# Performance work log

Hardware: AMD Instinct MI355X
Metric: run time of the kernel (lower is better)

The kernel has to match this reference:

```python
import jax, jax.numpy as jnp
import numpy as np

EPS = 1e-5

def setup_inputs() -> dict:
    key = jax.random.key(0)
    ks = jax.random.split(key, 5)
    B, C_clip, Hc, Wc = 8, 768, 24, 24
    C_rs, Hr, Wr = 256, 64, 64
    clip_feat = jax.random.normal(ks[0], (B, C_clip, Hc, Wc), dtype=jnp.float32)
    rs_feat = jax.random.normal(ks[1], (B, C_rs, Hr, Wr), dtype=jnp.float32)
    ln_gamma = jnp.ones((C_clip,), dtype=jnp.float32)
    ln_beta = jnp.zeros((C_clip,), dtype=jnp.float32)
    W = jax.random.normal(ks[2], (C_rs, C_clip), dtype=jnp.float32) * (1.0 / np.sqrt(C_clip))
    b = jax.random.normal(ks[3], (C_rs,), dtype=jnp.float32) * 0.01
    alpha = jnp.array([0.5], dtype=jnp.float32)
    return {"clip_feat": clip_feat, "rs_feat": rs_feat, "ln_gamma": ln_gamma,
            "ln_beta": ln_beta, "W": W, "b": b, "alpha": alpha}

def reference(clip_feat, rs_feat, ln_gamma, ln_beta, W, b, alpha):
    B, C_clip, Hc, Wc = clip_feat.shape
    _, C_rs, Hr, Wr = rs_feat.shape
    # tokens: [B, N_clip, C_clip]
    clip_flat = clip_feat.reshape(B, C_clip, Hc * Wc).transpose(0, 2, 1)
    mu = jnp.mean(clip_flat, axis=-1, keepdims=True)
    var = jnp.var(clip_flat, axis=-1, keepdims=True)
    clip_norm = (clip_flat - mu) * jax.lax.rsqrt(var + EPS) * ln_gamma + ln_beta
    # projection to rs_dim: [B, N_clip, C_rs]
    clip_proj = jnp.einsum('bnc,dc->bnd', clip_norm, W) + b
    # rs tokens: [B, N_rs, C_rs]
    rs_flat = rs_feat.reshape(B, C_rs, Hr * Wr).transpose(0, 2, 1)
    # attn_map: [B, N_clip, N_rs], softmax over N_clip (axis=1)
    attn = jnp.einsum('bnd,bmd->bnm', clip_proj, rs_flat)
    attn = jax.nn.softmax(attn, axis=1)
    # attended: [B, N_rs, C_rs]
    attended = jnp.einsum('bnm,bnd->bmd', attn, clip_proj)
    attended = attended.transpose(0, 2, 1).reshape(B, C_rs, Hr, Wr)
    return rs_feat + alpha * attended
```

## Files before the change

### kernel.cpp

```cpp
#include <hip/hip_runtime.h>
#include <hip/hip_bf16.h>

#define EPSF 1e-5f
#define SM_OFF 60.0f

typedef short short8 __attribute__((ext_vector_type(8)));
typedef float f32x4 __attribute__((ext_vector_type(4)));

__device__ __forceinline__ short f2bf(float x) {
    __hip_bfloat16 h = __float2bfloat16(x);
    return reinterpret_cast<short&>(h);
}
__device__ __forceinline__ float bf2f(short s) {
    __hip_bfloat16 h = reinterpret_cast<__hip_bfloat16&>(s);
    return __bfloat162float(h);
}
__device__ __forceinline__ unsigned int pk2(float lo, float hi) {
    return (unsigned int)(unsigned short)f2bf(lo)
         | ((unsigned int)(unsigned short)f2bf(hi) << 16);
}
__device__ __forceinline__ void gload_lds16(const short* g, short* lds) {
    __builtin_amdgcn_global_load_lds(
        (const __attribute__((address_space(1))) unsigned int*)g,
        (__attribute__((address_space(3))) unsigned int*)lds,
        16, 0, 0);
}

__global__ __launch_bounds__(256) void w_pack_kernel(
    const float* __restrict__ W,
    short* __restrict__ Wp_hi,
    short* __restrict__ Wp_lo)
{
    int t = blockIdx.x * 256 + threadIdx.x;
    int l15 = t & 15;
    int g   = (t >> 4) & 3;
    int kt  = (t >> 6) % 24;
    int nt  = t / 1536;
    const float* src = W + (size_t)(16 * nt + l15) * 768 + 32 * kt + 8 * g;
    short8 h8, l8;
    #pragma unroll
    for (int j = 0; j < 8; ++j) {
        float w = src[j];
        short h = f2bf(w);
        h8[j] = h;
        l8[j] = f2bf(w - bf2f(h));
    }
    *reinterpret_cast<short8*>(Wp_hi + (size_t)t * 8) = h8;
    *reinterpret_cast<short8*>(Wp_lo + (size_t)t * 8) = l8;
}

__global__ __launch_bounds__(512) void ln_proj_kernel(
    const float* __restrict__ clip,
    const float* __restrict__ gamma,
    const float* __restrict__ beta,
    const short* __restrict__ Wp_hi,
    const short* __restrict__ Wp_lo,
    const float* __restrict__ bias,
    short* __restrict__ proj,
    short* __restrict__ projT)
{
    __shared__ short xh[16][776];
    __shared__ short xl[16][776];
    __shared__ float redA[8][16];
    __shared__ float redB[8][16];
    __shared__ float muS[16], rsS[16];

    const int tid = threadIdx.x;
    const int bb = blockIdx.x >> 1;
    const int dh = blockIdx.x & 1;
    const int b  = bb / 36;
    const int n0 = (bb % 36) * 16;
    const int nl = tid & 15;
    const int cg = tid >> 4;
    const int w  = tid >> 6;
    const int l  = tid & 63;
    const int l15 = l & 15;
    const int g  = l >> 4;

    const float* base = clip + (size_t)b * 768 * 576 + n0 + nl;

    float x[24];
    float s1 = 0.f, s2 = 0.f;
    #pragma unroll
    for (int i = 0; i < 24; ++i) {
        x[i] = base[(size_t)(cg + 32 * i) * 576];
        s1 += x[i]; s2 += x[i] * x[i];
    }
    s1 += __shfl_xor(s1, 16); s2 += __shfl_xor(s2, 16);
    s1 += __shfl_xor(s1, 32); s2 += __shfl_xor(s2, 32);
    if (g == 0) { redA[w][l15] = s1; redB[w][l15] = s2; }
    __syncthreads();
    if (tid < 16) {
        float a = 0.f, q = 0.f;
        #pragma unroll
        for (int k = 0; k < 8; ++k) { a += redA[k][tid]; q += redB[k][tid]; }
        float mu = a * (1.f / 768.f);
        float var = q * (1.f / 768.f) - mu * mu;
        muS[tid] = mu; rsS[tid] = rsqrtf(var + EPSF);
    }
    __syncthreads();
    {
        float mu = muS[nl], rsg = rsS[nl];
        #pragma unroll
        for (int i = 0; i < 24; ++i) {
            int c = cg + 32 * i;
            float y = (x[i] - mu) * rsg * gamma[c] + beta[c];
            short hh = f2bf(y);
            xh[nl][c] = hh;
            xl[nl][c] = f2bf(y - bf2f(hh));
        }
    }
    __syncthreads();

    const int nt = 8 * dh + w;
    f32x4 acc = f32x4{0.f, 0.f, 0.f, 0.f};
    for (int kt = 0; kt < 24; ++kt) {
        short8 ah = *reinterpret_cast<const short8*>(&xh[l15][32 * kt + 8 * g]);
        short8 al = *reinterpret_cast<const short8*>(&xl[l15][32 * kt + 8 * g]);
        size_t off = ((size_t)((nt * 24 + kt) * 64 + l)) * 8;
        short8 bh = *reinterpret_cast<const short8*>(Wp_hi + off);
        short8 bl = *reinterpret_cast<const short8*>(Wp_lo + off);
        acc = __builtin_amdgcn_mfma_f32_16x16x32_bf16(ah, bh, acc, 0, 0, 0);
        acc = __builtin_amdgcn_mfma_f32_16x16x32_bf16(al, bh, acc, 0, 0, 0);
        acc = __builtin_amdgcn_mfma_f32_16x16x32_bf16(ah, bl, acc, 0, 0, 0);
    }

    {
        int d = 16 * nt + l15;
        float bb2 = bias[d];
        #pragma unroll
        for (int r = 0; r < 4; ++r) {
            int tok = n0 + 4 * g + r;
            short v = f2bf(acc[r] + bb2);
            proj[((size_t)b * 576 + tok) * 256 + d] = v;
            projT[((size_t)b * 256 + d) * 576 + tok] = v;
        }
    }
}

__global__ __launch_bounds__(256, 2) void attn_kernel(
    const short* __restrict__ proj,
    const short* __restrict__ projT,
    const float* __restrict__ rs,
    const float* __restrict__ alpha_p,
    float* __restrict__ out)
{
    __shared__ short Ks[64][256];
    __shared__ short VT[256][64];
    __shared__ unsigned int Ps[4][16][36];

    const int tid = threadIdx.x;
    const int b  = blockIdx.x & 7;
    const int q0 = (blockIdx.x >> 3) << 6;
    const int w   = tid >> 6;
    const int l   = tid & 63;
    const int l15 = l & 15;
    const int g   = l >> 4;
    const int qg  = q0 + 16 * w + l15;

    const short* kbase  = proj  + (size_t)b * 576 * 256;
    const short* ktbase = projT + (size_t)b * 256 * 576;
    const float* rbase  = rs + (size_t)b * 256 * 4096;
    float* obase = out + (size_t)b * 256 * 4096;

    short8 qf[8];
    #pragma unroll
    for (int dc = 0; dc < 8; ++dc) {
        short8 v;
        #pragma unroll
        for (int j = 0; j < 8; ++j)
            v[j] = f2bf(rbase[(size_t)(32 * dc + 8 * g + j) * 4096 + qg]);
        qf[dc] = v;
    }

    f32x4 acc[16];
    #pragma unroll
    for (int dt = 0; dt < 16; ++dt) acc[dt] = f32x4{0.f, 0.f, 0.f, 0.f};
    float rsum = 0.f;

    auto STAGE = [&](int c) {
        #pragma unroll
        for (int i = 0; i < 8; ++i) {
            int row0 = 16 * w + 2 * i;
            int rr = row0 + (l >> 5);
            const short* src = kbase + ((size_t)(64 * c + rr) << 8)
                             + ((((l & 31) ^ (rr & 7))) << 3);
            gload_lds16(src, &Ks[row0][0]);
        }
        #pragma unroll
        for (int i = 0; i < 8; ++i) {
            int d0 = 64 * w + 8 * i;
            int d = d0 + (l >> 3);
            const short* src = ktbase + (size_t)d * 576 + 64 * c
                             + (((l & 7) ^ (d & 7)) << 3);
            gload_lds16(src, &VT[d0][0]);
        }
    };

    STAGE(0);
    __syncthreads();

    for (int c = 0; c < 9; ++c) {
        f32x4 s[4];
        #pragma unroll
        for (int kt = 0; kt < 4; ++kt) s[kt] = f32x4{0.f, 0.f, 0.f, 0.f};
        __builtin_amdgcn_s_setprio(1);
        #pragma unroll
        for (int dc = 0; dc < 8; ++dc) {
            int sw = (((4 * dc + g) ^ (l15 & 7))) * 8;
            #pragma unroll
            for (int kt = 0; kt < 4; ++kt) {
                short8 kf = *reinterpret_cast<const short8*>(&Ks[16 * kt + l15][sw]);
                s[kt] = __builtin_amdgcn_mfma_f32_16x16x32_bf16(kf, qf[dc], s[kt], 0, 0, 0);
            }
        }
        __builtin_amdgcn_s_setprio(0);

        float p[16];
        #pragma unroll
        for (int kt = 0; kt < 4; ++kt)
            #pragma unroll
            for (int r = 0; r < 4; ++r) {
                p[4 * kt + r] = __expf(s[kt][r] - SM_OFF);
                rsum += p[4 * kt + r];
            }
        #pragma unroll
        for (int kt = 0; kt < 4; ++kt)
            *reinterpret_cast<uint2*>(&Ps[w][l15][8 * kt + 2 * g]) =
                uint2{pk2(p[4 * kt + 0], p[4 * kt + 1]),
                      pk2(p[4 * kt + 2], p[4 * kt + 3])};

        short8 pf0 = *reinterpret_cast<const short8*>(&Ps[w][l15][4 * g]);
        short8 pf1 = *reinterpret_cast<const short8*>(&Ps[w][l15][16 + 4 * g]);
        __builtin_amdgcn_s_setprio(1);
        #pragma unroll
        for (int dt = 0; dt < 16; ++dt) {
            short8 vf0 = *reinterpret_cast<const short8*>(
                &VT[16 * dt + l15][((g ^ (l15 & 7))) << 3]);
            short8 vf1 = *reinterpret_cast<const short8*>(
                &VT[16 * dt + l15][(((4 + g) ^ (l15 & 7))) << 3]);
            acc[dt] = __builtin_amdgcn_mfma_f32_16x16x32_bf16(vf0, pf0, acc[dt], 0, 0, 0);
            acc[dt] = __builtin_amdgcn_mfma_f32_16x16x32_bf16(vf1, pf1, acc[dt], 0, 0, 0);
        }
        __builtin_amdgcn_s_setprio(0);

        __syncthreads();
        if (c < 8) {
            STAGE(c + 1);
            __syncthreads();
        }
    }

    rsum += __shfl_xor(rsum, 16);
    rsum += __shfl_xor(rsum, 32);
    float inv = alpha_p[0] / rsum;

    #pragma unroll
    for (int dt = 0; dt < 16; ++dt) {
        #pragma unroll
        for (int r = 0; r < 4; ++r) {
            int d = 16 * dt + 4 * g + r;
            size_t idx = (size_t)d * 4096 + qg;
            obase[idx] = rbase[idx] + acc[dt][r] * inv;
        }
    }
}

extern "C" void kernel_launch(void* const* d_in, const int* in_sizes, int n_in,
                              void* d_out, int out_size, void* d_ws, size_t ws_size,
                              hipStream_t stream)
{
    const float* clip  = (const float*)d_in[0];
    const float* rsf   = (const float*)d_in[1];
    const float* gamma = (const float*)d_in[2];
    const float* beta  = (const float*)d_in[3];
    const float* W     = (const float*)d_in[4];
    const float* bias  = (const float*)d_in[5];
    const float* alpha = (const float*)d_in[6];
    float* out = (float*)d_out;

    char* ws = (char*)d_ws;
    short* Wp_hi = (short*)ws;
    short* Wp_lo = (short*)(ws + 393216);
    short* proj  = (short*)(ws + 786432);
    short* projT = (short*)(ws + 3145728);

    hipLaunchKernelGGL(w_pack_kernel, dim3(96), dim3(256), 0, stream, W, Wp_hi, Wp_lo);
    hipLaunchKernelGGL(ln_proj_kernel, dim3(576), dim3(512), 0, stream,
                       clip, gamma, beta, Wp_hi, Wp_lo, bias, proj, projT);
    hipLaunchKernelGGL(attn_kernel, dim3(512), dim3(256), 0, stream,
                       proj, projT, rsf, alpha, out);
}
```

Before: 68.41 us.

## Switch attention to 32x32 MFMA with query/key wave split and staggered staging

Recasts the attention kernel from 16x16x32 to 32x32x16 bf16 MFMA tiles. The four waves become a 2x2 grid: query halves by key halves for QK^T, and query halves by output-channel halves for PV. Probabilities are shared between waves through shared memory, and row sums are combined through a small buffer at the end. K and V staging for the next chunk are split so each overlaps the other phase's compute, and Q loads are issued after the first stage starts. The intent is to cut LDS fragment reads and barrier stalls per FLOP, at the cost of extra cross-wave synchronisation and higher register pressure from the larger accumulators.

```diff
diff --git a/kernel.cpp b/kernel.cpp
--- a/kernel.cpp
+++ b/kernel.cpp
@@ -6,6 +6,7 @@
 
 typedef short short8 __attribute__((ext_vector_type(8)));
 typedef float f32x4 __attribute__((ext_vector_type(4)));
+typedef float f32x16 __attribute__((ext_vector_type(16)));
 
 __device__ __forceinline__ short f2bf(float x) {
     __hip_bfloat16 h = __float2bfloat16(x);
@@ -147,46 +148,36 @@
 {
     __shared__ short Ks[64][256];
     __shared__ short VT[256][64];
-    __shared__ unsigned int Ps[4][16][36];
+    __shared__ unsigned int Pb[2][32][36];
+    __shared__ float Rb[2][2][32];
 
     const int tid = threadIdx.x;
     const int b  = blockIdx.x & 7;
     const int q0 = (blockIdx.x >> 3) << 6;
     const int w   = tid >> 6;
     const int l   = tid & 63;
-    const int l15 = l & 15;
-    const int g   = l >> 4;
-    const int qg  = q0 + 16 * w + l15;
+    const int l31 = l & 31;
+    const int hi  = l >> 5;
+    const int qh  = w >> 1;
+    const int kh  = w & 1;
+    const int qg  = q0 + 32 * qh + l31;
 
     const short* kbase  = proj  + (size_t)b * 576 * 256;
     const short* ktbase = projT + (size_t)b * 256 * 576;
     const float* rbase  = rs + (size_t)b * 256 * 4096;
     float* obase = out + (size_t)b * 256 * 4096;
 
-    short8 qf[8];
-    #pragma unroll
-    for (int dc = 0; dc < 8; ++dc) {
-        short8 v;
-        #pragma unroll
-        for (int j = 0; j < 8; ++j)
-            v[j] = f2bf(rbase[(size_t)(32 * dc + 8 * g + j) * 4096 + qg]);
-        qf[dc] = v;
-    }
-
-    f32x4 acc[16];
-    #pragma unroll
-    for (int dt = 0; dt < 16; ++dt) acc[dt] = f32x4{0.f, 0.f, 0.f, 0.f};
-    float rsum = 0.f;
-
-    auto STAGE = [&](int c) {
+    auto STAGE_K = [&](int c) {
         #pragma unroll
         for (int i = 0; i < 8; ++i) {
             int row0 = 16 * w + 2 * i;
             int rr = row0 + (l >> 5);
             const short* src = kbase + ((size_t)(64 * c + rr) << 8)
-                             + ((((l & 31) ^ (rr & 7))) << 3);
+                             + ((((l & 31) ^ (rr & 15))) << 3);
             gload_lds16(src, &Ks[row0][0]);
         }
+    };
+    auto STAGE_V = [&](int c) {
         #pragma unroll
         for (int i = 0; i < 8; ++i) {
             int d0 = 64 * w + 8 * i;
@@ -197,69 +188,95 @@
         }
     };
 
-    STAGE(0);
-    __syncthreads();
-
+    STAGE_K(0);
+    STAGE_V(0);
+
+    short8 qf[16];
+    #pragma unroll
+    for (int st = 0; st < 16; ++st) {
+        short8 v;
+        #pragma unroll
+        for (int j = 0; j < 8; ++j)
+            v[j] = f2bf(rbase[(size_t)(16 * st + 8 * hi + j) * 4096 + qg]);
+        qf[st] = v;
+    }
+
+    f32x16 acc[4];
+    #pragma unroll
+    for (int dt = 0; dt < 4; ++dt)
+        #pragma unroll
+        for (int r = 0; r < 16; ++r) acc[dt][r] = 0.f;
+    float rsum = 0.f;
+
+    __syncthreads();
+
+    const int krow = 32 * kh + l31;
     for (int c = 0; c < 9; ++c) {
-        f32x4 s[4];
-        #pragma unroll
-        for (int kt = 0; kt < 4; ++kt) s[kt] = f32x4{0.f, 0.f, 0.f, 0.f};
+        f32x16 sA, sB;
+        #pragma unroll
+        for (int r = 0; r < 16; ++r) { sA[r] = 0.f; sB[r] = 0.f; }
         __builtin_amdgcn_s_setprio(1);
         #pragma unroll
-        for (int dc = 0; dc < 8; ++dc) {
-            int sw = (((4 * dc + g) ^ (l15 & 7))) * 8;
+        for (int st = 0; st < 8; ++st) {
+            int pos = ((2 * st + hi) ^ (krow & 15)) << 3;
+            short8 kf = *reinterpret_cast<const short8*>(&Ks[krow][pos]);
+            sA = __builtin_amdgcn_mfma_f32_32x32x16_bf16(kf, qf[st], sA, 0, 0, 0);
+        }
+        #pragma unroll
+        for (int st = 8; st < 16; ++st) {
+            int pos = ((2 * st + hi) ^ (krow & 15)) << 3;
+            short8 kf = *reinterpret_cast<const short8*>(&Ks[krow][pos]);
+            sB = __builtin_amdgcn_mfma_f32_32x32x16_bf16(kf, qf[st], sB, 0, 0, 0);
+        }
+        __builtin_amdgcn_s_setprio(0);
+
+        float p[16];
+        #pragma unroll
+        for (int r = 0; r < 16; ++r) {
+            p[r] = __expf(sA[r] + sB[r] - SM_OFF);
+            rsum += p[r];
+        }
+        #pragma unroll
+        for (int m = 0; m < 4; ++m) {
+            int slot = 2 * m + hi + 8 * kh;
+            int swz  = slot ^ (2 * (l31 & 7));
+            *reinterpret_cast<uint2*>(&Pb[qh][l31][2 * swz]) =
+                uint2{pk2(p[4 * m + 0], p[4 * m + 1]),
+                      pk2(p[4 * m + 2], p[4 * m + 3])};
+        }
+
+        __syncthreads();
+        if (c < 8) STAGE_K(c + 1);
+
+        __builtin_amdgcn_s_setprio(1);
+        #pragma unroll
+        for (int ks = 0; ks < 4; ++ks) {
+            int es = (4 * ks + 2 * hi) ^ (2 * (l31 & 7));
+            short8 pf = *reinterpret_cast<const short8*>(&Pb[qh][l31][2 * es]);
             #pragma unroll
-            for (int kt = 0; kt < 4; ++kt) {
-                short8 kf = *reinterpret_cast<const short8*>(&Ks[16 * kt + l15][sw]);
-                s[kt] = __builtin_amdgcn_mfma_f32_16x16x32_bf16(kf, qf[dc], s[kt], 0, 0, 0);
+            for (int dt = 0; dt < 4; ++dt) {
+                int d = 128 * kh + 32 * dt + l31;
+                int pos = ((2 * ks + hi) ^ (d & 7)) << 3;
+                short8 vf = *reinterpret_cast<const short8*>(&VT[d][pos]);
+                acc[dt] = __builtin_amdgcn_mfma_f32_32x32x16_bf16(vf, pf, acc[dt], 0, 0, 0);
             }
         }
         __builtin_amdgcn_s_setprio(0);
 
-        float p[16];
-        #pragma unroll
-        for (int kt = 0; kt < 4; ++kt)
-            #pragma unroll
-            for (int r = 0; r < 4; ++r) {
-                p[4 * kt + r] = __expf(s[kt][r] - SM_OFF);
-                rsum += p[4 * kt + r];
-            }
-        #pragma unroll
-        for (int kt = 0; kt < 4; ++kt)
-            *reinterpret_cast<uint2*>(&Ps[w][l15][8 * kt + 2 * g]) =
-                uint2{pk2(p[4 * kt + 0], p[4 * kt + 1]),
-                      pk2(p[4 * kt + 2], p[4 * kt + 3])};
-
-        short8 pf0 = *reinterpret_cast<const short8*>(&Ps[w][l15][4 * g]);
-        short8 pf1 = *reinterpret_cast<const short8*>(&Ps[w][l15][16 + 4 * g]);
-        __builtin_amdgcn_s_setprio(1);
-        #pragma unroll
-        for (int dt = 0; dt < 16; ++dt) {
-            short8 vf0 = *reinterpret_cast<const short8*>(
-                &VT[16 * dt + l15][((g ^ (l15 & 7))) << 3]);
-            short8 vf1 = *reinterpret_cast<const short8*>(
-                &VT[16 * dt + l15][(((4 + g) ^ (l15 & 7))) << 3]);
-            acc[dt] = __builtin_amdgcn_mfma_f32_16x16x32_bf16(vf0, pf0, acc[dt], 0, 0, 0);
-            acc[dt] = __builtin_amdgcn_mfma_f32_16x16x32_bf16(vf1, pf1, acc[dt], 0, 0, 0);
-        }
-        __builtin_amdgcn_s_setprio(0);
-
         __syncthreads();
-        if (c < 8) {
-            STAGE(c + 1);
-            __syncthreads();
-        }
-    }
-
-    rsum += __shfl_xor(rsum, 16);
+        if (c < 8) STAGE_V(c + 1);
+    }
+
     rsum += __shfl_xor(rsum, 32);
-    float inv = alpha_p[0] / rsum;
-
-    #pragma unroll
-    for (int dt = 0; dt < 16; ++dt) {
-        #pragma unroll
-        for (int r = 0; r < 4; ++r) {
-            int d = 16 * dt + 4 * g + r;
+    if (hi == 0) Rb[qh][kh][l31] = rsum;
+    __syncthreads();
+    float inv = alpha_p[0] / (Rb[qh][0][l31] + Rb[qh][1][l31]);
+
+    #pragma unroll
+    for (int dt = 0; dt < 4; ++dt) {
+        #pragma unroll
+        for (int r = 0; r < 16; ++r) {
+            int d = 128 * kh + 32 * dt + (r & 3) + 8 * (r >> 2) + 4 * hi;
             size_t idx = (size_t)d * 4096 + qg;
             obase[idx] = rbase[idx] + acc[dt][r] * inv;
         }
```

Result: no change. 68.86 us (+0.7%).
